# Kernel optimization log

Hardware: AMD Instinct MI355X
Metric: run time of the kernel (lower is better)

## Reference

```python
import jax, jax.numpy as jnp
import numpy as np

N_ENT = 100000   # n_entities
N_HE = 20000     # n_hyperedges
D = 128          # embed_dim (in_dim == out_dim)
NNZ_A = 1600000  # nnz of A_in (~16 per row)
NNZ_H = 1000000  # nnz of each hyperedge incidence matrix


def spmm(rows, cols, vals, x, n_rows):
    """COO sparse (n_rows, n_cols) @ dense x (n_cols, D) -> (n_rows, D)."""
    msgs = vals[:, None] * x[cols]  # [nnz, D] gather + scale
    return jax.ops.segment_sum(msgs, rows, num_segments=n_rows)


def setup_inputs() -> dict:
    key = jax.random.key(0)
    ks = jax.random.split(key, 18)
    ego = jax.random.normal(ks[0], (N_ENT, D), dtype=jnp.float32)
    a_rows = jax.random.randint(ks[1], (NNZ_A,), 0, N_ENT)
    a_cols = jax.random.randint(ks[2], (NNZ_A,), 0, N_ENT)
    a_vals = jax.random.uniform(ks[3], (NNZ_A,), dtype=jnp.float32)
    p1_rows = jax.random.randint(ks[4], (NNZ_H,), 0, N_HE)
    p1_cols = jax.random.randint(ks[5], (NNZ_H,), 0, N_ENT)
    p1_vals = jax.random.uniform(ks[6], (NNZ_H,), dtype=jnp.float32)
    p2_rows = jax.random.randint(ks[7], (NNZ_H,), 0, N_ENT)
    p2_cols = jax.random.randint(ks[8], (NNZ_H,), 0, N_HE)
    p2_vals = jax.random.uniform(ks[9], (NNZ_H,), dtype=jnp.float32)
    l1_rows = jax.random.randint(ks[10], (NNZ_H,), 0, N_HE)
    l1_cols = jax.random.randint(ks[11], (NNZ_H,), 0, N_ENT)
    l1_vals = jax.random.uniform(ks[12], (NNZ_H,), dtype=jnp.float32)
    l2_rows = jax.random.randint(ks[13], (NNZ_H,), 0, N_ENT)
    l2_cols = jax.random.randint(ks[14], (NNZ_H,), 0, N_HE)
    l2_vals = jax.random.uniform(ks[15], (NNZ_H,), dtype=jnp.float32)
    W1 = jax.random.normal(ks[16], (D, D), dtype=jnp.float32) * 0.05
    b1 = jnp.zeros((D,), dtype=jnp.float32)
    W2 = jax.random.normal(ks[17], (D, D), dtype=jnp.float32) * 0.05
    b2 = jnp.zeros((D,), dtype=jnp.float32)
    return dict(ego=ego, a_rows=a_rows, a_cols=a_cols, a_vals=a_vals,
                p1_rows=p1_rows, p1_cols=p1_cols, p1_vals=p1_vals,
                p2_rows=p2_rows, p2_cols=p2_cols, p2_vals=p2_vals,
                l1_rows=l1_rows, l1_cols=l1_cols, l1_vals=l1_vals,
                l2_rows=l2_rows, l2_cols=l2_cols, l2_vals=l2_vals,
                W1=W1, b1=b1, W2=W2, b2=b2)


def reference(ego, a_rows, a_cols, a_vals,
              p1_rows, p1_cols, p1_vals,
              p2_rows, p2_cols, p2_vals,
              l1_rows, l1_cols, l1_vals,
              l2_rows, l2_cols, l2_vals,
              W1, b1, W2, b2):
    # side = A_in @ ego
    side = spmm(a_rows, a_cols, a_vals, ego, N_ENT)
    # proj = norm_proj2 @ (norm_proj1 @ ego)
    proj = spmm(p2_rows, p2_cols, p2_vals,
                spmm(p1_rows, p1_cols, p1_vals, ego, N_HE), N_ENT)
    # lib = norm_lib2 @ (norm_lib1 @ ego)
    lib = spmm(l2_rows, l2_cols, l2_vals,
               spmm(l1_rows, l1_cols, l1_vals, ego, N_HE), N_ENT)
    side = side + proj + lib
    # bi-interaction aggregator (PyTorch Linear: x @ W.T + b), LeakyReLU slope 0.01
    sum_emb = jax.nn.leaky_relu((ego + side) @ W1.T + b1)
    bi_emb = jax.nn.leaky_relu((ego * side) @ W2.T + b2)
    # attention=True -> sum of both branches; dropout is identity in eval
    return sum_emb + bi_emb
```

## Files before the change

### kernel.cpp

```cpp
#include <hip/hip_runtime.h>

#define N_ENT 100000
#define N_HE  20000
#define DD    128

#define XROW_H1 100000
#define XROW_H2 120000
#define NXROWS  140000

#define RP_S2  0
#define RP_P1  100001
#define RP_L1  120002
#define RP_LEN 140803

#define NB 354
#define TILE 3072
#define EPT  12

typedef float f32x4 __attribute__((ext_vector_type(4)));
typedef short bf16x8 __attribute__((ext_vector_type(8)));

__device__ __forceinline__ int bucket_region(int b) {
    return (b < 196) ? 0 : (b < 275) ? 1 : 2;
}
__device__ __forceinline__ int reg_shift(int r)      { return r == 0 ? 9 : 8; }
__device__ __forceinline__ int reg_bucketbase(int r) { return r == 0 ? 0 : r == 1 ? 196 : 275; }
__device__ __forceinline__ int reg_cap(int r)        { return r == 0 ? 19968 : 13824; }
__device__ __forceinline__ long long reg_arenabase(int r) {
    return r == 0 ? 0LL : r == 1 ? 3913728LL : 5005824LL;
}
__device__ __forceinline__ int reg_rpbase(int r)     { return r == 0 ? RP_S2 : r == 1 ? RP_P1 : RP_L1; }
__device__ __forceinline__ int reg_rows(int r)       { return r == 0 ? 100000 : 20000; }

__device__ __forceinline__ unsigned short f2bf(float f) {
    unsigned u = __float_as_uint(f);
    unsigned r = (u + 0x7fffu + ((u >> 16) & 1u)) >> 16;
    return (unsigned short)r;
}
__device__ __forceinline__ unsigned pack_bf16(float a, float b) {
    return (unsigned)f2bf(a) | ((unsigned)f2bf(b) << 16);
}
__device__ __forceinline__ float lrelu(float x) { return x > 0.0f ? x : 0.01f * x; }
__device__ __forceinline__ float i8f(unsigned u, int b) {
    return (float)((int)(u << (24 - 8 * b)) >> 24);
}

__global__ __launch_bounds__(256) void quant_ego_kernel(
    const float* __restrict__ ego, unsigned* __restrict__ xq,
    float* __restrict__ xs)
{
    int row = (blockIdx.x * 256 + threadIdx.x) >> 5;
    if (row >= N_ENT) return;
    int l = threadIdx.x & 31;
    const float4 v = *(const float4*)(ego + (long long)row * DD + l * 4);
    float m = fmaxf(fmaxf(fabsf(v.x), fabsf(v.y)), fmaxf(fabsf(v.z), fabsf(v.w)));
    for (int d = 1; d < 32; d <<= 1) m = fmaxf(m, __shfl_xor(m, d, 32));
    float inv = (m > 0.0f) ? 127.0f / m : 0.0f;
    int q0 = __float2int_rn(v.x * inv);
    int q1 = __float2int_rn(v.y * inv);
    int q2 = __float2int_rn(v.z * inv);
    int q3 = __float2int_rn(v.w * inv);
    unsigned pk = (q0 & 255) | ((q1 & 255) << 8) | ((q2 & 255) << 16) | ((q3 & 255) << 24);
    xq[row * 32 + l] = pk;
    if (l == 0) xs[row] = m * (1.0f / 127.0f);
}

struct BuildArgs {
    const int*   rows[5];
    const int*   cols[5];
    const float* vals[5];
    int nnzbase[6];
};

__device__ __forceinline__ int seg_bbase(int s)  { return (s == 1) ? 196 : (s == 3) ? 275 : 0; }
__device__ __forceinline__ int seg_shift2(int s) { return (s == 1 || s == 3) ? 8 : 9; }
__device__ __forceinline__ int seg_colofs(int s) { return (s == 2) ? XROW_H1 : (s == 4) ? XROW_H2 : 0; }

__device__ __forceinline__ void seg_of(int i, const int* nnzbase, int& seg, int& li) {
    int s = 0;
    s += (i >= nnzbase[1]);
    s += (i >= nnzbase[2]);
    s += (i >= nnzbase[3]);
    s += (i >= nnzbase[4]);
    seg = s; li = i - nnzbase[s];
}

__global__ __launch_bounds__(256, 4) void partition_kernel(
    BuildArgs a, int* __restrict__ gcursor, int2* __restrict__ arena)
{
    __shared__ int2 staging[TILE];
    __shared__ unsigned short posb[TILE];
    __shared__ int  hist[NB];
    __shared__ int  excl[NB + 1];
    __shared__ int  cursor[NB];
    __shared__ int  gofs[NB];

    const int t = threadIdx.x;
    const int tile_base = blockIdx.x * TILE;
    const int total = a.nnzbase[5];
    int tile_n = total - tile_base;
    if (tile_n > TILE) tile_n = TILE;
    if (tile_n <= 0) return;

    for (int i = t; i < NB; i += 256) hist[i] = 0;
    __syncthreads();

    int pk[EPT];
#pragma unroll
    for (int q = 0; q < EPT; ++q) {
        int j = t + q * 256;
        pk[q] = -1;
        if (j < tile_n) {
            int i = tile_base + j;
            int seg, li; seg_of(i, a.nnzbase, seg, li);
            int row = a.rows[seg][li];
            int sh = seg_shift2(seg);
            int b = seg_bbase(seg) + (row >> sh);
            int rl = row & ((1 << sh) - 1);
            pk[q] = (b << 9) | rl;
            atomicAdd(&hist[b], 1);
        }
    }
    __syncthreads();

    if (t < 64) {
        int carry = 0;
        for (int base = 0; base < NB; base += 64) {
            int idx = base + t;
            int v = (idx < NB) ? hist[idx] : 0;
            int inc = v;
            for (int d = 1; d < 64; d <<= 1) {
                int u = __shfl_up(inc, d, 64);
                if (t >= d) inc += u;
            }
            if (idx < NB) excl[idx] = carry + inc - v;
            carry += __shfl(inc, 63, 64);
        }
        if (t == 0) excl[NB] = carry;
    }
    __syncthreads();

    for (int b = t; b < NB; b += 256) {
        int c = hist[b];
        int e = excl[b];
        int gb = (c > 0) ? atomicAdd(&gcursor[b], c) : 0;
        cursor[b] = e;
        gofs[b] = gb - e;
    }
    __syncthreads();

#pragma unroll
    for (int q = 0; q < EPT; ++q) {
        int j = t + q * 256;
        if (j < tile_n) {
            int i = tile_base + j;
            int seg, li; seg_of(i, a.nnzbase, seg, li);
            int colp = a.cols[seg][li] + seg_colofs(seg);
            float v = a.vals[seg][li];
            int b = pk[q] >> 9;
            int rl = pk[q] & 511;
            int pos = atomicAdd(&cursor[b], 1);
            staging[pos] = make_int2((rl << 18) | colp, __float_as_int(v));
        }
    }
    __syncthreads();

    for (int b = t; b < NB; b += 256) {
        int lo = excl[b], hi = excl[b + 1];
        for (int p = lo; p < hi; ++p) posb[p] = (unsigned short)b;
    }
    __syncthreads();

    for (int p = t; p < tile_n; p += 256) {
        int b = posb[p];
        int reg = bucket_region(b);
        long long slot = reg_arenabase(reg) + (long long)(b - reg_bucketbase(reg)) * reg_cap(reg);
        arena[slot + gofs[b] + p] = staging[p];
    }
}

__global__ __launch_bounds__(512) void bucket_scan_kernel(
    const int* __restrict__ gcursor, int* __restrict__ bbase, int* __restrict__ rp)
{
    __shared__ int tmp[512];
    int t = threadIdx.x;
    int v = (t < NB) ? gcursor[t] : 0;
    tmp[t] = v;
    __syncthreads();
    for (int d = 1; d < 512; d <<= 1) {
        int u = (t >= d) ? tmp[t - d] : 0;
        __syncthreads();
        tmp[t] += u;
        __syncthreads();
    }
    if (t < NB) bbase[t] = tmp[t] - v;
    if (t == 196) rp[RP_S2 + 100000] = tmp[t] - v;
    if (t == 275) rp[RP_P1 + 20000]  = tmp[t] - v;
    if (t == NB - 1) rp[RP_L1 + 20000] = tmp[t];
}

__global__ __launch_bounds__(256) void bucket_sort_kernel(
    const int* __restrict__ gcursor, const int* __restrict__ bbase,
    const int2* __restrict__ arena, int2* __restrict__ cv, int* __restrict__ rp)
{
    __shared__ int hist[512];
    __shared__ int excl[512];
    __shared__ int wsum[4];

    const int b = blockIdx.x;
    const int t = threadIdx.x;
    const int reg = bucket_region(b);
    const int sh = reg_shift(reg);
    const int stride = 1 << sh;
    const int lb = b - reg_bucketbase(reg);
    const int row_base_local = lb << sh;
    int nrows = reg_rows(reg) - row_base_local;
    if (nrows > stride) nrows = stride;
    const long long slot = reg_arenabase(reg) + (long long)lb * reg_cap(reg);
    const int count = gcursor[b];
    const int fbase = bbase[b];

    for (int i = t; i < 512; i += 256) hist[i] = 0;
    __syncthreads();

    for (int j = t; j < count; j += 256) {
        int key = arena[slot + j].x;
        atomicAdd(&hist[key >> 18], 1);
    }
    __syncthreads();

    {
        const int lane = t & 63, wave = t >> 6;
        int v0 = hist[t * 2], v1 = hist[t * 2 + 1];
        int s = v0 + v1;
        int inc = s;
        for (int d = 1; d < 64; d <<= 1) {
            int u = __shfl_up(inc, d, 64);
            if (lane >= d) inc += u;
        }
        if (lane == 63) wsum[wave] = inc;
        __syncthreads();
        int woff = 0;
        for (int w = 0; w < wave; ++w) woff += wsum[w];
        int run = woff + inc - s;
        excl[t * 2] = run;
        excl[t * 2 + 1] = run + v0;
    }
    __syncthreads();

    const int grow0 = reg_rpbase(reg) + row_base_local;
    for (int r = t; r < nrows; r += 256)
        rp[grow0 + r] = fbase + excl[r];
    __syncthreads();

    for (int j = t; j < count; j += 256) {
        int2 e = arena[slot + j];
        int r = e.x >> 18;
        int c = e.x & 0x3FFFF;
        int pos = atomicAdd(&excl[r], 1);
        cv[fbase + pos] = make_int2(c, e.y);
    }
}

__device__ __forceinline__ void walk_row8(
    const int2* __restrict__ cv, int start, int end, int lane,
    const unsigned* __restrict__ xq, const float* __restrict__ xs, float* acc)
{
    const int g = lane >> 3;
    const int s = lane & 7;

    for (int sb = start; sb < end; sb += 64) {
        int nn = end - sb; if (nn > 64) nn = 64;
        int2 mycv = make_int2(0, 0);
        float myv = 0.0f;
        if (lane < nn) {
            mycv = cv[sb + lane];
            myv = __int_as_float(mycv.y) * xs[mycv.x];
        }
        const int nn1 = nn - 1;
#pragma unroll 2
        for (int jb = 0; jb < nn; jb += 8) {
            int idx  = jb + g;
            int idxc = idx < nn1 ? idx : nn1;
            int   cs = __shfl(mycv.x, idxc, 64);
            float vs = __shfl(myv, idxc, 64);
            vs = (idx <= nn1) ? vs : 0.0f;
            const uint4 u = *reinterpret_cast<const uint4*>(xq + cs * 32 + s * 4);
#pragma unroll
            for (int w = 0; w < 4; ++w) {
                unsigned uw = (&u.x)[w];
                acc[w * 4 + 0] = fmaf(vs, i8f(uw, 0), acc[w * 4 + 0]);
                acc[w * 4 + 1] = fmaf(vs, i8f(uw, 1), acc[w * 4 + 1]);
                acc[w * 4 + 2] = fmaf(vs, i8f(uw, 2), acc[w * 4 + 2]);
                acc[w * 4 + 3] = fmaf(vs, i8f(uw, 3), acc[w * 4 + 3]);
            }
        }
    }
}

__device__ __forceinline__ void reduce_groups8(float* acc)
{
#pragma unroll
    for (int e = 0; e < 16; ++e) {
        acc[e] += __shfl_xor(acc[e], 8, 64);
        acc[e] += __shfl_xor(acc[e], 16, 64);
        acc[e] += __shfl_xor(acc[e], 32, 64);
    }
}

__global__ __launch_bounds__(256) void spmm_stage1_kernel(
    const int* __restrict__ rp, const int2* __restrict__ cv,
    unsigned* __restrict__ xq, float* __restrict__ xs)
{
    int wid = (blockIdx.x * 256 + threadIdx.x) >> 6;
    int lane = threadIdx.x & 63;
    if (wid >= 2 * N_HE) return;
    int rbase, xrow;
    if (wid < N_HE) { rbase = RP_P1 + wid;           xrow = XROW_H1 + wid; }
    else            { rbase = RP_L1 + (wid - N_HE);  xrow = XROW_H2 + (wid - N_HE); }

    float acc[16];
#pragma unroll
    for (int e = 0; e < 16; ++e) acc[e] = 0.0f;
    walk_row8(cv, rp[rbase], rp[rbase + 1], lane, xq, xs, acc);
    reduce_groups8(acc);

    float m = 0.0f;
#pragma unroll
    for (int e = 0; e < 16; ++e) m = fmaxf(m, fabsf(acc[e]));
    m = fmaxf(m, __shfl_xor(m, 1, 64));
    m = fmaxf(m, __shfl_xor(m, 2, 64));
    m = fmaxf(m, __shfl_xor(m, 4, 64));
    float inv = (m > 0.0f) ? 127.0f / m : 0.0f;

    if (lane < 8) {
        uint4 o;
#pragma unroll
        for (int w = 0; w < 4; ++w) {
            int q0 = __float2int_rn(acc[w * 4 + 0] * inv);
            int q1 = __float2int_rn(acc[w * 4 + 1] * inv);
            int q2 = __float2int_rn(acc[w * 4 + 2] * inv);
            int q3 = __float2int_rn(acc[w * 4 + 3] * inv);
            (&o.x)[w] = (q0 & 255) | ((q1 & 255) << 8) | ((q2 & 255) << 16) | ((q3 & 255) << 24);
        }
        *reinterpret_cast<uint4*>(xq + xrow * 32 + lane * 4) = o;
        if (lane == 0) xs[xrow] = m * (1.0f / 127.0f);
    }
}

__global__ __launch_bounds__(256) void spmm_stage2_kernel(
    const int* __restrict__ rp, const int2* __restrict__ cv,
    const unsigned* __restrict__ xq, const float* __restrict__ xs,
    float* __restrict__ side)
{
    int wid = (blockIdx.x * 256 + threadIdx.x) >> 6;
    int lane = threadIdx.x & 63;
    if (wid >= N_ENT) return;

    float acc[16];
#pragma unroll
    for (int e = 0; e < 16; ++e) acc[e] = 0.0f;
    walk_row8(cv, rp[wid], rp[wid + 1], lane, xq, xs, acc);
    reduce_groups8(acc);

    if (lane < 8) {
        float* yp = side + (long long)wid * DD + lane * 16;
#pragma unroll
        for (int w = 0; w < 4; ++w)
            *reinterpret_cast<float4*>(yp + w * 4) =
                make_float4(acc[w * 4], acc[w * 4 + 1], acc[w * 4 + 2], acc[w * 4 + 3]);
    }
}

union BfFrag { unsigned u[4]; bf16x8 v; };

__global__ __launch_bounds__(512, 4) void dense_mfma_kernel(
    const float* __restrict__ ego, const float* __restrict__ side,
    const float* __restrict__ W1, const float* __restrict__ b1,
    const float* __restrict__ W2, const float* __restrict__ b2,
    float* __restrict__ out)
{
    __shared__ unsigned Wb1[8192];
    __shared__ unsigned Wb2[8192];

    const int tid = threadIdx.x;

    for (int idx = tid; idx < 8192; idx += 512) {
        int row = idx >> 6, pc = idx & 63;
        unsigned pk1 = pack_bf16(W1[row * 128 + pc * 2], W1[row * 128 + pc * 2 + 1]);
        unsigned pk2 = pack_bf16(W2[row * 128 + pc * 2], W2[row * 128 + pc * 2 + 1]);
        int boff = row * 256 + ((pc * 4) ^ ((row & 7) << 4));
        *(unsigned*)((char*)Wb1 + boff) = pk1;
        *(unsigned*)((char*)Wb2 + boff) = pk2;
    }
    __syncthreads();

    const int wave = tid >> 6;
    const int lane = tid & 63;
    const int m    = lane & 15;
    const int kg   = lane >> 4;

    float bs[8], bb[8];
#pragma unroll
    for (int c = 0; c < 8; ++c) {
        bs[c] = b1[c * 16 + m];
        bb[c] = b2[c * 16 + m];
    }

    for (int wt = blockIdx.x * 8 + wave; wt < 6250; wt += gridDim.x * 8) {
        const long long r0 = (long long)(wt * 16 + m) * DD;

        f32x4 accS[8], accB[8];
#pragma unroll
        for (int c = 0; c < 8; ++c) { accS[c] = (f32x4)0.0f; accB[c] = (f32x4)0.0f; }

#pragma unroll 1
        for (int kk = 0; kk < 4; ++kk) {
            const int kb = kk * 32 + kg * 8;

            float4 ea = *(const float4*)(ego  + r0 + kb);
            float4 eb = *(const float4*)(ego  + r0 + kb + 4);
            float4 sa = *(const float4*)(side + r0 + kb);
            float4 sb = *(const float4*)(side + r0 + kb + 4);

            BfFrag aS, aB;
            aS.u[0] = pack_bf16(ea.x + sa.x, ea.y + sa.y);
            aS.u[1] = pack_bf16(ea.z + sa.z, ea.w + sa.w);
            aS.u[2] = pack_bf16(eb.x + sb.x, eb.y + sb.y);
            aS.u[3] = pack_bf16(eb.z + sb.z, eb.w + sb.w);
            aB.u[0] = pack_bf16(ea.x * sa.x, ea.y * sa.y);
            aB.u[1] = pack_bf16(ea.z * sa.z, ea.w * sa.w);
            aB.u[2] = pack_bf16(eb.x * sb.x, eb.y * sb.y);
            aB.u[3] = pack_bf16(eb.z * sb.z, eb.w * sb.w);

#pragma unroll
            for (int c = 0; c < 8; ++c) {
                int wrow = c * 16 + m;
                int boff = wrow * 256 + ((kk * 64 + (kg << 4)) ^ ((wrow & 7) << 4));
                bf16x8 w1 = *(const bf16x8*)((const char*)Wb1 + boff);
                bf16x8 w2 = *(const bf16x8*)((const char*)Wb2 + boff);
                accS[c] = __builtin_amdgcn_mfma_f32_16x16x32_bf16(aS.v, w1, accS[c], 0, 0, 0);
                accB[c] = __builtin_amdgcn_mfma_f32_16x16x32_bf16(aB.v, w2, accB[c], 0, 0, 0);
            }
        }

#pragma unroll
        for (int c = 0; c < 8; ++c) {
#pragma unroll
            for (int q = 0; q < 4; ++q) {
                int orow = wt * 16 + kg * 4 + q;
                out[(long long)orow * DD + c * 16 + m] =
                    lrelu(accS[c][q] + bs[c]) + lrelu(accB[c][q] + bb[c]);
            }
        }
    }
}

extern "C" void kernel_launch(void* const* d_in, const int* in_sizes, int n_in,
                              void* d_out, int out_size, void* d_ws, size_t ws_size,
                              hipStream_t stream)
{
    const float* ego = (const float*)d_in[0];
    const float* W1  = (const float*)d_in[16];
    const float* b1  = (const float*)d_in[17];
    const float* W2  = (const float*)d_in[18];
    const float* b2  = (const float*)d_in[19];

    BuildArgs a;
    a.rows[0] = (const int*)d_in[1];  a.cols[0] = (const int*)d_in[2];  a.vals[0] = (const float*)d_in[3];
    a.rows[1] = (const int*)d_in[4];  a.cols[1] = (const int*)d_in[5];  a.vals[1] = (const float*)d_in[6];
    a.rows[2] = (const int*)d_in[7];  a.cols[2] = (const int*)d_in[8];  a.vals[2] = (const float*)d_in[9];
    a.rows[3] = (const int*)d_in[10]; a.cols[3] = (const int*)d_in[11]; a.vals[3] = (const float*)d_in[12];
    a.rows[4] = (const int*)d_in[13]; a.cols[4] = (const int*)d_in[14]; a.vals[4] = (const float*)d_in[15];
    int nnz[5] = { in_sizes[1], in_sizes[4], in_sizes[7], in_sizes[10], in_sizes[13] };
    a.nnzbase[0] = 0;
    for (int s = 0; s < 5; ++s) a.nnzbase[s + 1] = a.nnzbase[s] + nnz[s];
    const int total = a.nnzbase[5];

    char* p = (char*)d_ws;
    float*    side    = (float*)p;
    int2*     arena   = (int2*)p;         p += (size_t)N_ENT * DD * 4;
    unsigned* xq      = (unsigned*)p;     p += (size_t)140032 * 32 * 4;
    float*    xs      = (float*)p;        p += (size_t)140032 * 4;
    int2*     cv      = (int2*)p;         p += (size_t)total * 8;
    int*      rp      = (int*)p;          p += 141056 * 4;
    int*      gcursor = (int*)p;          p += 512 * 4;
    int*      bbase   = (int*)p;          p += 512 * 4;

    hipMemsetAsync(gcursor, 0, NB * sizeof(int), stream);
    quant_ego_kernel<<<(N_ENT * 32 + 255) / 256, 256, 0, stream>>>(ego, xq, xs);
    const int nblk_part = (total + TILE - 1) / TILE;
    partition_kernel<<<nblk_part, 256, 0, stream>>>(a, gcursor, arena);
    bucket_scan_kernel<<<1, 512, 0, stream>>>(gcursor, bbase, rp);
    bucket_sort_kernel<<<NB, 256, 0, stream>>>(gcursor, bbase, arena, cv, rp);

    spmm_stage1_kernel<<<(2 * N_HE) / 4, 256, 0, stream>>>(rp, cv, xq, xs);
    spmm_stage2_kernel<<<N_ENT / 4, 256, 0, stream>>>(rp, cv, xq, xs, side);

    dense_mfma_kernel<<<782, 512, 0, stream>>>(ego, side, W1, b1, W2, b2, (float*)d_out);
}
```

Before: 332.5 us.

## Use uniform 256-row buckets, smaller partition tiles, and cache col/val in registers

```diff
diff --git a/kernel.cpp b/kernel.cpp
--- a/kernel.cpp
+++ b/kernel.cpp
@@ -6,28 +6,25 @@
 
 #define XROW_H1 100000
 #define XROW_H2 120000
-#define NXROWS  140000
 
 #define RP_S2  0
 #define RP_P1  100001
 #define RP_L1  120002
-#define RP_LEN 140803
-
-#define NB 354
-#define TILE 3072
-#define EPT  12
+
+#define NB 549
+#define TILE 2048
+#define EPT  8
 
 typedef float f32x4 __attribute__((ext_vector_type(4)));
 typedef short bf16x8 __attribute__((ext_vector_type(8)));
 
 __device__ __forceinline__ int bucket_region(int b) {
-    return (b < 196) ? 0 : (b < 275) ? 1 : 2;
-}
-__device__ __forceinline__ int reg_shift(int r)      { return r == 0 ? 9 : 8; }
-__device__ __forceinline__ int reg_bucketbase(int r) { return r == 0 ? 0 : r == 1 ? 196 : 275; }
-__device__ __forceinline__ int reg_cap(int r)        { return r == 0 ? 19968 : 13824; }
+    return (b < 391) ? 0 : (b < 470) ? 1 : 2;
+}
+__device__ __forceinline__ int reg_bucketbase(int r) { return r == 0 ? 0 : r == 1 ? 391 : 470; }
+__device__ __forceinline__ int reg_cap(int r)        { return r == 0 ? 10240 : 13824; }
 __device__ __forceinline__ long long reg_arenabase(int r) {
-    return r == 0 ? 0LL : r == 1 ? 3913728LL : 5005824LL;
+    return r == 0 ? 0LL : r == 1 ? 4003840LL : 5095936LL;
 }
 __device__ __forceinline__ int reg_rpbase(int r)     { return r == 0 ? RP_S2 : r == 1 ? RP_P1 : RP_L1; }
 __device__ __forceinline__ int reg_rows(int r)       { return r == 0 ? 100000 : 20000; }
@@ -72,8 +69,7 @@
     int nnzbase[6];
 };
 
-__device__ __forceinline__ int seg_bbase(int s)  { return (s == 1) ? 196 : (s == 3) ? 275 : 0; }
-__device__ __forceinline__ int seg_shift2(int s) { return (s == 1 || s == 3) ? 8 : 9; }
+__device__ __forceinline__ int seg_bbase(int s)  { return (s == 1) ? 391 : (s == 3) ? 470 : 0; }
 __device__ __forceinline__ int seg_colofs(int s) { return (s == 2) ? XROW_H1 : (s == 4) ? XROW_H2 : 0; }
 
 __device__ __forceinline__ void seg_of(int i, const int* nnzbase, int& seg, int& li) {
@@ -85,7 +81,7 @@
     seg = s; li = i - nnzbase[s];
 }
 
-__global__ __launch_bounds__(256, 4) void partition_kernel(
+__global__ __launch_bounds__(256, 5) void partition_kernel(
     BuildArgs a, int* __restrict__ gcursor, int2* __restrict__ arena)
 {
     __shared__ int2 staging[TILE];
@@ -105,7 +101,9 @@
     for (int i = t; i < NB; i += 256) hist[i] = 0;
     __syncthreads();
 
-    int pk[EPT];
+    int   pk[EPT];
+    int   pcol[EPT];
+    float pval[EPT];
 #pragma unroll
     for (int q = 0; q < EPT; ++q) {
         int j = t + q * 256;
@@ -114,10 +112,10 @@
             int i = tile_base + j;
             int seg, li; seg_of(i, a.nnzbase, seg, li);
             int row = a.rows[seg][li];
-            int sh = seg_shift2(seg);
-            int b = seg_bbase(seg) + (row >> sh);
-            int rl = row & ((1 << sh) - 1);
-            pk[q] = (b << 9) | rl;
+            pcol[q] = a.cols[seg][li] + seg_colofs(seg);
+            pval[q] = a.vals[seg][li];
+            int b = seg_bbase(seg) + (row >> 8);
+            pk[q] = (b << 8) | (row & 255);
             atomicAdd(&hist[b], 1);
         }
     }
@@ -141,33 +139,24 @@
     __syncthreads();
 
     for (int b = t; b < NB; b += 256) {
-        int c = hist[b];
-        int e = excl[b];
+        int e  = excl[b];
+        int hi = excl[b + 1];
+        int c  = hi - e;
         int gb = (c > 0) ? atomicAdd(&gcursor[b], c) : 0;
         cursor[b] = e;
         gofs[b] = gb - e;
+        for (int p = e; p < hi; ++p) posb[p] = (unsigned short)b;
     }
     __syncthreads();
 
 #pragma unroll
     for (int q = 0; q < EPT; ++q) {
-        int j = t + q * 256;
-        if (j < tile_n) {
-            int i = tile_base + j;
-            int seg, li; seg_of(i, a.nnzbase, seg, li);
-            int colp = a.cols[seg][li] + seg_colofs(seg);
-            float v = a.vals[seg][li];
-            int b = pk[q] >> 9;
-            int rl = pk[q] & 511;
+        if (pk[q] >= 0) {
+            int b  = pk[q] >> 8;
+            int rl = pk[q] & 255;
             int pos = atomicAdd(&cursor[b], 1);
-            staging[pos] = make_int2((rl << 18) | colp, __float_as_int(v));
-        }
-    }
-    __syncthreads();
-
-    for (int b = t; b < NB; b += 256) {
-        int lo = excl[b], hi = excl[b + 1];
-        for (int p = lo; p < hi; ++p) posb[p] = (unsigned short)b;
+            staging[pos] = make_int2((rl << 18) | pcol[q], __float_as_int(pval[q]));
+        }
     }
     __syncthreads();
 
@@ -179,23 +168,23 @@
     }
 }
 
-__global__ __launch_bounds__(512) void bucket_scan_kernel(
+__global__ __launch_bounds__(1024) void bucket_scan_kernel(
     const int* __restrict__ gcursor, int* __restrict__ bbase, int* __restrict__ rp)
 {
-    __shared__ int tmp[512];
+    __shared__ int tmp[1024];
     int t = threadIdx.x;
     int v = (t < NB) ? gcursor[t] : 0;
     tmp[t] = v;
     __syncthreads();
-    for (int d = 1; d < 512; d <<= 1) {
+    for (int d = 1; d < 1024; d <<= 1) {
         int u = (t >= d) ? tmp[t - d] : 0;
         __syncthreads();
         tmp[t] += u;
         __syncthreads();
     }
     if (t < NB) bbase[t] = tmp[t] - v;
-    if (t == 196) rp[RP_S2 + 100000] = tmp[t] - v;
-    if (t == 275) rp[RP_P1 + 20000]  = tmp[t] - v;
+    if (t == 391) rp[RP_S2 + 100000] = tmp[t] - v;
+    if (t == 470) rp[RP_P1 + 20000]  = tmp[t] - v;
     if (t == NB - 1) rp[RP_L1 + 20000] = tmp[t];
 }
 
@@ -203,24 +192,22 @@
     const int* __restrict__ gcursor, const int* __restrict__ bbase,
     const int2* __restrict__ arena, int2* __restrict__ cv, int* __restrict__ rp)
 {
-    __shared__ int hist[512];
-    __shared__ int excl[512];
+    __shared__ int hist[256];
+    __shared__ int excl[256];
     __shared__ int wsum[4];
 
     const int b = blockIdx.x;
     const int t = threadIdx.x;
     const int reg = bucket_region(b);
-    const int sh = reg_shift(reg);
-    const int stride = 1 << sh;
     const int lb = b - reg_bucketbase(reg);
-    const int row_base_local = lb << sh;
+    const int row_base_local = lb << 8;
     int nrows = reg_rows(reg) - row_base_local;
-    if (nrows > stride) nrows = stride;
+    if (nrows > 256) nrows = 256;
     const long long slot = reg_arenabase(reg) + (long long)lb * reg_cap(reg);
     const int count = gcursor[b];
     const int fbase = bbase[b];
 
-    for (int i = t; i < 512; i += 256) hist[i] = 0;
+    hist[t] = 0;
     __syncthreads();
 
     for (int j = t; j < count; j += 256) {
@@ -231,9 +218,8 @@
 
     {
         const int lane = t & 63, wave = t >> 6;
-        int v0 = hist[t * 2], v1 = hist[t * 2 + 1];
-        int s = v0 + v1;
-        int inc = s;
+        int v = hist[t];
+        int inc = v;
         for (int d = 1; d < 64; d <<= 1) {
             int u = __shfl_up(inc, d, 64);
             if (lane >= d) inc += u;
@@ -242,23 +228,19 @@
         __syncthreads();
         int woff = 0;
         for (int w = 0; w < wave; ++w) woff += wsum[w];
-        int run = woff + inc - s;
-        excl[t * 2] = run;
-        excl[t * 2 + 1] = run + v0;
-    }
-    __syncthreads();
-
-    const int grow0 = reg_rpbase(reg) + row_base_local;
-    for (int r = t; r < nrows; r += 256)
-        rp[grow0 + r] = fbase + excl[r];
+        excl[t] = woff + inc - v;
+    }
+    __syncthreads();
+
+    if (t < nrows)
+        rp[reg_rpbase(reg) + row_base_local + t] = fbase + excl[t];
     __syncthreads();
 
     for (int j = t; j < count; j += 256) {
         int2 e = arena[slot + j];
         int r = e.x >> 18;
-        int c = e.x & 0x3FFFF;
         int pos = atomicAdd(&excl[r], 1);
-        cv[fbase + pos] = make_int2(c, e.y);
+        cv[fbase + pos] = make_int2(e.x & 0x3FFFF, e.y);
     }
 }
 
@@ -484,14 +466,14 @@
     float*    xs      = (float*)p;        p += (size_t)140032 * 4;
     int2*     cv      = (int2*)p;         p += (size_t)total * 8;
     int*      rp      = (int*)p;          p += 141056 * 4;
-    int*      gcursor = (int*)p;          p += 512 * 4;
-    int*      bbase   = (int*)p;          p += 512 * 4;
+    int*      gcursor = (int*)p;          p += 1024 * 4;
+    int*      bbase   = (int*)p;          p += 1024 * 4;
 
     hipMemsetAsync(gcursor, 0, NB * sizeof(int), stream);
     quant_ego_kernel<<<(N_ENT * 32 + 255) / 256, 256, 0, stream>>>(ego, xq, xs);
     const int nblk_part = (total + TILE - 1) / TILE;
     partition_kernel<<<nblk_part, 256, 0, stream>>>(a, gcursor, arena);
-    bucket_scan_kernel<<<1, 512, 0, stream>>>(gcursor, bbase, rp);
+    bucket_scan_kernel<<<1, 1024, 0, stream>>>(gcursor, bbase, rp);
     bucket_sort_kernel<<<NB, 256, 0, stream>>>(gcursor, bbase, arena, cv, rp);
 
     spmm_stage1_kernel<<<(2 * N_HE) / 4, 256, 0, stream>>>(rp, cv, xq, xs);
```

Measured after the change: 314.6 us. 5.4% less time.
